# Performance work log

Hardware: AMD Instinct MI355X
Metric: run time of the kernel (lower is better)

Reference implementation:

```python
import jax, jax.numpy as jnp
import numpy as np

B, T, N, C_IN, C_HID, C_OUT = 1, 128, 50000, 16, 32, 8
E = 1_600_000
K = 2  # Chebyshev order


def setup_inputs() -> dict:
    key = jax.random.key(0)
    ks = jax.random.split(key, 12)
    X = jax.random.normal(ks[0], (B, T, N, C_IN), dtype=jnp.float32)
    edge_index = jax.random.randint(ks[1], (2, E), 0, N, dtype=jnp.int64)

    def mk_w(k, cin, cout):
        return jax.random.normal(k, (K, cin, cout), dtype=jnp.float32) / np.float32(np.sqrt(cin * K))

    inp = {"X": X, "edge_index": edge_index}
    names = ["xz", "hz", "xr", "hr", "xh", "hh"]
    for i, nm in enumerate(names):
        cin = C_IN if nm[0] == "x" else C_HID
        inp["W_" + nm] = mk_w(ks[2 + i], cin, C_HID)
        inp["b_" + nm] = jnp.zeros((C_HID,), jnp.float32)
    inp["fc_w"] = jax.random.normal(ks[10], (C_HID, C_OUT), jnp.float32) / np.float32(np.sqrt(C_HID))
    inp["fc_b"] = jnp.zeros((C_OUT,), jnp.float32)
    return inp


def _lap_edge_weights(edge_index, n):
    # ChebConv sym normalization with lambda_max=2: L_hat = -D^{-1/2} A D^{-1/2}, zero diag
    src, dst = edge_index[0], edge_index[1]
    deg = jax.ops.segment_sum(jnp.ones(src.shape, jnp.float32), src, num_segments=n)
    dinv = jnp.where(deg > 0, jax.lax.rsqrt(jnp.maximum(deg, 1.0)), 0.0)
    return -dinv[src] * dinv[dst]


def reference(X, edge_index, W_xz, b_xz, W_hz, b_hz, W_xr, b_xr, W_hr, b_hr,
              W_xh, b_xh, W_hh, b_hh, fc_w, fc_b):
    Ntot = B * N
    src, dst = edge_index[0], edge_index[1]
    w = _lap_edge_weights(edge_index, Ntot)  # [E]

    def agg(x):  # Tx_1 = L_hat @ x, irregular gather/scatter over edges
        return jax.ops.segment_sum(w[:, None] * x[src], dst, num_segments=Ntot)

    def cheb(x, W, b):  # K=2 Chebyshev conv
        return x @ W[0] + agg(x) @ W[1] + b

    def step(h, x_t):  # GConvGRU cell
        Z = jax.nn.sigmoid(cheb(x_t, W_xz, b_xz) + cheb(h, W_hz, b_hz))
        R = jax.nn.sigmoid(cheb(x_t, W_xr, b_xr) + cheb(h, W_hr, b_hr))
        Ht = jnp.tanh(cheb(x_t, W_xh, b_xh) + cheb(h * R, W_hh, b_hh))
        h = Z * h + (1.0 - Z) * Ht
        return h, h

    xs = jnp.swapaxes(X, 0, 1).reshape(T, Ntot, C_IN)  # [T, B*N, C_in]
    h0 = jnp.zeros((Ntot, C_HID), jnp.float32)
    _, hs = jax.lax.scan(step, h0, xs)                 # [T, B*N, H]
    outs = hs.reshape(T, B, N, C_HID).swapaxes(0, 1)   # [B, T, N, H]
    return outs @ fc_w + fc_b                           # [B, T, N, C_out]
```

## Files before the change

### kernel.cpp

```cpp
#include <hip/hip_runtime.h>
#include <cstdint>

#define NN   50000
#define TT   128
#define EE   1600000
#define CIN  16
#define CH   32
#define COUT 8

__device__ __forceinline__ float rlane(float v, int k) {
  return __int_as_float(__builtin_amdgcn_readlane(__float_as_int(v), k));
}
__device__ __forceinline__ float xhalf(float v) {
  return __shfl_xor(v, 32, 64);
}
__device__ __forceinline__ float sigf(float x) {
  return 1.0f / (1.0f + __expf(-x));
}
__device__ __forceinline__ float tanh_fast(float x) {
  x = fminf(fmaxf(x, -30.0f), 30.0f);
  float e = __expf(2.0f * x);
  return (e - 1.0f) / (e + 1.0f);
}

__global__ void k_flag(const int* __restrict__ idx, int* __restrict__ flag) {
  if (threadIdx.x == 0) {
    int m = 1;
    for (int i = 1; i <= 32; ++i)
      if (idx[2 * i + 1] != 0) m = 0;
    flag[0] = m;
  }
}

__global__ void k_zero_i(int* __restrict__ p, int n) {
  int i = blockIdx.x * blockDim.x + threadIdx.x;
  if (i < n) p[i] = 0;
}
__global__ void k_zero_f(float* __restrict__ p, int n) {
  int i = blockIdx.x * blockDim.x + threadIdx.x;
  if (i < n) p[i] = 0.0f;
}

__global__ void k_deg(const int* __restrict__ idx, int* __restrict__ deg_s,
                      int* __restrict__ deg_d, const int* __restrict__ flag) {
  int e = blockIdx.x * blockDim.x + threadIdx.x;
  if (e >= EE) return;
  int m = flag[0];
  int s = m ? idx[2 * e] : idx[e];
  int d = m ? idx[2 * (EE + e)] : idx[EE + e];
  atomicAdd(&deg_s[s], 1);
  atomicAdd(&deg_d[d], 1);
}

__global__ void k_dinv(const int* __restrict__ deg_s, float* __restrict__ dinv) {
  int i = blockIdx.x * blockDim.x + threadIdx.x;
  if (i < NN) {
    int d = deg_s[i];
    dinv[i] = (d > 0) ? rsqrtf((float)d) : 0.0f;
  }
}

__global__ void k_scan(const int* __restrict__ deg, int* __restrict__ row_ptr,
                       int* __restrict__ cursor) {
  __shared__ int part[1024];
  int tid = threadIdx.x;
  const int chunk = (NN + 1023) / 1024;
  int b = tid * chunk;
  int e = b + chunk; if (e > NN) e = NN;
  int s = 0;
  for (int j = b; j < e; ++j) s += deg[j];
  part[tid] = s;
  __syncthreads();
  for (int off = 1; off < 1024; off <<= 1) {
    int v = part[tid];
    int add = (tid >= off) ? part[tid - off] : 0;
    __syncthreads();
    part[tid] = v + add;
    __syncthreads();
  }
  int run = (tid > 0) ? part[tid - 1] : 0;
  for (int j = b; j < e; ++j) {
    row_ptr[j] = run; cursor[j] = run;
    run += deg[j];
  }
  if (tid == 1023) row_ptr[NN] = part[1023];
}

__global__ void k_fill(const int* __restrict__ idx, const float* __restrict__ dinv,
                       int* __restrict__ cursor, int* __restrict__ col,
                       float* __restrict__ wgt, const int* __restrict__ flag) {
  int e = blockIdx.x * blockDim.x + threadIdx.x;
  if (e >= EE) return;
  int m = flag[0];
  int s = m ? idx[2 * e] : idx[e];
  int d = m ? idx[2 * (EE + e)] : idx[EE + e];
  int p = atomicAdd(&cursor[d], 1);
  col[p] = s;
  wgt[p] = -dinv[s] * dinv[d];
}


__global__ __launch_bounds__(256, 4) void kx(
    const float* __restrict__ Xt,
    const int* __restrict__ row_ptr, const int* __restrict__ col,
    const float* __restrict__ wgt,
    const float* __restrict__ W_xz, const float* __restrict__ b_xz,
    const float* __restrict__ b_hz,
    const float* __restrict__ W_xr, const float* __restrict__ b_xr,
    const float* __restrict__ b_hr,
    const float* __restrict__ W_xh, const float* __restrict__ b_xh,
    const float* __restrict__ b_hh,
    float* __restrict__ Gx) {
  const int lane = threadIdx.x & 63;
  const int g = lane >> 5;
  const int c = lane & 31;
  const int ci = c & 15;
  const int wid = (blockIdx.x * blockDim.x + threadIdx.x) >> 6;
  const int nw = (gridDim.x * blockDim.x) >> 6;

  const float* Wzr = g ? W_xr : W_xz;
  float w0[CIN], w1[CIN], wh0[CIN], wh1[CIN];
#pragma unroll
  for (int k = 0; k < CIN; ++k) {
    w0[k]  = Wzr[k * CH + c];
    w1[k]  = Wzr[CIN * CH + k * CH + c];
    wh0[k] = W_xh[k * CH + c];
    wh1[k] = W_xh[CIN * CH + k * CH + c];
  }
  const float bzr = g ? (b_xr[c] + b_hr[c]) : (b_xz[c] + b_hz[c]);
  const float bh  = b_xh[c] + b_hh[c];

  for (int i = wid; i < NN; i += nw) {
    const int iu = __builtin_amdgcn_readfirstlane(i);
    const int e0 = __builtin_amdgcn_readfirstlane(row_ptr[iu]);
    const int e1 = __builtin_amdgcn_readfirstlane(row_ptr[iu + 1]);
    const int deg = e1 - e0;
    const int len0 = (deg + 1) >> 1;
    const int s = e0 + (g ? len0 : 0);
    const int send = g ? e1 : (e0 + len0);

    float a0 = 0.f, a1 = 0.f, a2 = 0.f, a3 = 0.f;
    int j = s;
    for (; j + 4 <= send; j += 4) {
      int s0 = col[j], s1 = col[j + 1], s2 = col[j + 2], s3 = col[j + 3];
      float wA = wgt[j], wB = wgt[j + 1], wC = wgt[j + 2], wD = wgt[j + 3];
      a0 += wA * Xt[s0 * CIN + ci];
      a1 += wB * Xt[s1 * CIN + ci];
      a2 += wC * Xt[s2 * CIN + ci];
      a3 += wD * Xt[s3 * CIN + ci];
    }
    for (; j < send; ++j)
      a0 += wgt[j] * Xt[col[j] * CIN + ci];
    float axh = (a0 + a1) + (a2 + a3);
    float ax = axh + xhalf(axh);

    const float* xrow = Xt + (size_t)iu * CIN;
    float accA = bzr, accH = bh;
#pragma unroll
    for (int k = 0; k < CIN; ++k) {
      float xk = xrow[k];
      float axk = rlane(ax, k);
      accA += xk * w0[k] + axk * w1[k];
      accH += xk * wh0[k] + axk * wh1[k];
    }
    float* grow = Gx + (size_t)iu * 96;
    grow[g * CH + c] = accA;
    if (g == 0) grow[64 + c] = accH;
  }
}

__global__ __launch_bounds__(256, 4) void k1(
    const float* __restrict__ h,
    const int* __restrict__ row_ptr, const int* __restrict__ col,
    const float* __restrict__ wgt,
    const float* __restrict__ W_hz, const float* __restrict__ W_hr,
    const float* __restrict__ Gx,
    float* __restrict__ Zb, float* __restrict__ hrb) {
  const int lane = threadIdx.x & 63;
  const int g = lane >> 5;
  const int c = lane & 31;
  const int wid = (blockIdx.x * blockDim.x + threadIdx.x) >> 6;
  const int nw = (gridDim.x * blockDim.x) >> 6;

  const float* Wh = g ? W_hr : W_hz;
  float w0[CH], w1[CH];
#pragma unroll
  for (int k = 0; k < CH; ++k) {
    w0[k] = Wh[k * CH + c];
    w1[k] = Wh[CH * CH + k * CH + c];
  }

  for (int i = wid; i < NN; i += nw) {
    const int iu = __builtin_amdgcn_readfirstlane(i);
    const int e0 = __builtin_amdgcn_readfirstlane(row_ptr[iu]);
    const int e1 = __builtin_amdgcn_readfirstlane(row_ptr[iu + 1]);
    const int deg = e1 - e0;
    const int len0 = (deg + 1) >> 1;
    const int s = e0 + (g ? len0 : 0);
    const int send = g ? e1 : (e0 + len0);

    float a0 = 0.f, a1 = 0.f, a2 = 0.f, a3 = 0.f;
    int j = s;
    for (; j + 4 <= send; j += 4) {
      int s0 = col[j], s1 = col[j + 1], s2 = col[j + 2], s3 = col[j + 3];
      float wA = wgt[j], wB = wgt[j + 1], wC = wgt[j + 2], wD = wgt[j + 3];
      a0 += wA * h[s0 * CH + c];
      a1 += wB * h[s1 * CH + c];
      a2 += wC * h[s2 * CH + c];
      a3 += wD * h[s3 * CH + c];
    }
    for (; j < send; ++j)
      a0 += wgt[j] * h[col[j] * CH + c];
    float ahh = (a0 + a1) + (a2 + a3);
    float ah = ahh + xhalf(ahh);

    const float* hrow = h + (size_t)iu * CH;
    float acc = Gx[(size_t)iu * 96 + g * CH + c];
#pragma unroll
    for (int k = 0; k < CH; ++k) {
      float hk = hrow[k];
      float ahk = rlane(ah, k);
      acc += hk * w0[k] + ahk * w1[k];
    }
    float sg = sigf(acc);
    float hv = hrow[c];
    if (g == 0) Zb[(size_t)iu * CH + c] = sg;
    else        hrb[(size_t)iu * CH + c] = hv * sg;
  }
}

__global__ __launch_bounds__(256, 4) void k2(
    float* __restrict__ h, const float* __restrict__ hrb,
    const int* __restrict__ row_ptr, const int* __restrict__ col,
    const float* __restrict__ wgt,
    const float* __restrict__ W_hh,
    const float* __restrict__ fc_w, const float* __restrict__ fc_b,
    const float* __restrict__ Gx, const float* __restrict__ Zb,
    float* __restrict__ outT) {
  const int lane = threadIdx.x & 63;
  const int g = lane >> 5;
  const int c = lane & 31;
  const int wid = (blockIdx.x * blockDim.x + threadIdx.x) >> 6;
  const int nw = (gridDim.x * blockDim.x) >> 6;

  float w0[CH], w1[CH], fcw[CH];
#pragma unroll
  for (int k = 0; k < CH; ++k) {
    w0[k] = W_hh[k * CH + c];
    w1[k] = W_hh[CH * CH + k * CH + c];
    fcw[k] = fc_w[k * COUT + (c & 7)];
  }
  const float fb = fc_b[c & 7];

  for (int i = wid; i < NN; i += nw) {
    const int iu = __builtin_amdgcn_readfirstlane(i);
    const int e0 = __builtin_amdgcn_readfirstlane(row_ptr[iu]);
    const int e1 = __builtin_amdgcn_readfirstlane(row_ptr[iu + 1]);
    const int deg = e1 - e0;
    const int len0 = (deg + 1) >> 1;
    const int s = e0 + (g ? len0 : 0);
    const int send = g ? e1 : (e0 + len0);

    float a0 = 0.f, a1 = 0.f, a2 = 0.f, a3 = 0.f;
    int j = s;
    for (; j + 4 <= send; j += 4) {
      int s0 = col[j], s1 = col[j + 1], s2 = col[j + 2], s3 = col[j + 3];
      float wA = wgt[j], wB = wgt[j + 1], wC = wgt[j + 2], wD = wgt[j + 3];
      a0 += wA * hrb[s0 * CH + c];
      a1 += wB * hrb[s1 * CH + c];
      a2 += wC * hrb[s2 * CH + c];
      a3 += wD * hrb[s3 * CH + c];
    }
    for (; j < send; ++j)
      a0 += wgt[j] * hrb[col[j] * CH + c];
    float ahh = (a0 + a1) + (a2 + a3);
    float ahr = ahh + xhalf(ahh);

    const float* hrrow = hrb + (size_t)iu * CH;
    const float* hrow = h + (size_t)iu * CH;
    float acc = Gx[(size_t)iu * 96 + 64 + c];
#pragma unroll
    for (int k = 0; k < CH; ++k) {
      float hk = hrrow[k];
      float ahk = rlane(ahr, k);
      acc += hk * w0[k] + ahk * w1[k];
    }
    float ht = tanh_fast(acc);
    float zv = Zb[(size_t)iu * CH + c];
    float hv = hrow[c];
    float hn = zv * hv + (1.0f - zv) * ht;
    if (g == 0) h[(size_t)iu * CH + c] = hn;

    float o0 = fb, o1 = 0.f;
#pragma unroll
    for (int k = 0; k < CH; k += 2) {
      o0 += rlane(hn, k) * fcw[k];
      o1 += rlane(hn, k + 1) * fcw[k + 1];
    }
    float o = o0 + o1;
    if (lane < COUT) outT[(size_t)iu * COUT + lane] = o;
  }
}

extern "C" void kernel_launch(void* const* d_in, const int* in_sizes, int n_in,
                              void* d_out, int out_size, void* d_ws, size_t ws_size,
                              hipStream_t stream) {
  const float* X = (const float*)d_in[0];
  const int* idx = (const int*)d_in[1];
  const float* W_xz = (const float*)d_in[2];  const float* b_xz = (const float*)d_in[3];
  const float* W_hz = (const float*)d_in[4];  const float* b_hz = (const float*)d_in[5];
  const float* W_xr = (const float*)d_in[6];  const float* b_xr = (const float*)d_in[7];
  const float* W_hr = (const float*)d_in[8];  const float* b_hr = (const float*)d_in[9];
  const float* W_xh = (const float*)d_in[10]; const float* b_xh = (const float*)d_in[11];
  const float* W_hh = (const float*)d_in[12]; const float* b_hh = (const float*)d_in[13];
  const float* fc_w = (const float*)d_in[14]; const float* fc_b = (const float*)d_in[15];
  float* out = (float*)d_out;

  char* ws = (char*)d_ws;
  size_t off = 0;
  auto alloc = [&](size_t bytes) -> void* {
    void* p = ws + off;
    off = (off + bytes + 255) & ~(size_t)255;
    return p;
  };
  int* flag = (int*)alloc(4);
  int* deg_s = (int*)alloc((size_t)NN * 4);
  int* deg_d = (int*)alloc((size_t)NN * 4);
  int* row_ptr = (int*)alloc((size_t)(NN + 1) * 4);
  int* cursor = (int*)alloc((size_t)NN * 4);
  float* dinv = (float*)alloc((size_t)NN * 4);
  int* col = (int*)alloc((size_t)EE * 4);
  float* wgt = (float*)alloc((size_t)EE * 4);
  float* h = (float*)alloc((size_t)NN * CH * 4);
  float* hrb = (float*)alloc((size_t)NN * CH * 4);
  float* Zb = (float*)alloc((size_t)NN * CH * 4);
  float* Gx = (float*)alloc((size_t)NN * 96 * 4);

  k_flag<<<1, 64, 0, stream>>>(idx, flag);
  k_zero_i<<<(NN + 255) / 256, 256, 0, stream>>>(deg_s, NN);
  k_zero_i<<<(NN + 255) / 256, 256, 0, stream>>>(deg_d, NN);
  k_deg<<<(EE + 255) / 256, 256, 0, stream>>>(idx, deg_s, deg_d, flag);
  k_dinv<<<(NN + 255) / 256, 256, 0, stream>>>(deg_s, dinv);
  k_scan<<<1, 1024, 0, stream>>>(deg_d, row_ptr, cursor);
  k_fill<<<(EE + 255) / 256, 256, 0, stream>>>(idx, dinv, cursor, col, wgt, flag);
  k_zero_f<<<(NN * CH + 255) / 256, 256, 0, stream>>>(h, NN * CH);

  const int blocks = 3125;
  for (int t = 0; t < TT; ++t) {
    const float* Xt = X + (size_t)t * NN * CIN;
    float* outT = out + (size_t)t * NN * COUT;
    kx<<<blocks, 256, 0, stream>>>(Xt, row_ptr, col, wgt,
                                   W_xz, b_xz, b_hz, W_xr, b_xr, b_hr,
                                   W_xh, b_xh, b_hh, Gx);
    k1<<<blocks, 256, 0, stream>>>(h, row_ptr, col, wgt, W_hz, W_hr, Gx, Zb, hrb);
    k2<<<blocks, 256, 0, stream>>>(h, hrb, row_ptr, col, wgt, W_hh,
                                   fc_w, fc_b, Gx, Zb, outT);
  }
}
```

Measured before the change: 26.84 ms.

## Hoist input-side Chebyshev convs out of time loop and batch gathers

Adds a single kx_all kernel that computes the input-side gate preactivations for all 128 timesteps up front, processing four timesteps per edge traversal so the col/wgt reads are shared. It is used when the workspace can hold a full T×N×96 buffer, and it removes the kx launch from the recurrent loop. The edge-gather loops in k1/k2 are rewritten to load 16 indices and weights at a time with a clamped tail, which exposes more memory-level parallelism. The recurrent kernels now process two nodes per wave iteration with launch bounds lowered to 3 waves per SIMD. The cost is a buffer of about 2.4 GB, plus extra memory traffic to write Gx for every timestep and read it back later.

```diff
diff --git a/kernel.cpp b/kernel.cpp
--- a/kernel.cpp
+++ b/kernel.cpp
@@ -21,6 +21,35 @@
   x = fminf(fmaxf(x, -30.0f), 30.0f);
   float e = __expf(2.0f * x);
   return (e - 1.0f) / (e + 1.0f);
+}
+
+__device__ __forceinline__ float agg16(const float* __restrict__ mat,
+                                       const int* __restrict__ col,
+                                       const float* __restrict__ wgt,
+                                       int e0, int e1, int g, int c) {
+  const int deg = e1 - e0;
+  const int len0 = (deg + 1) >> 1;
+  const int s = e0 + (g ? len0 : 0);
+  const int send = g ? e1 : (e0 + len0);
+  float a[4] = {0.f, 0.f, 0.f, 0.f};
+  int j = s;
+  while (j < send) {
+    int cidx[16];
+    float wv[16];
+#pragma unroll
+    for (int k = 0; k < 16; ++k) {
+      int jk = j + k;
+      int sj = (jk < send) ? jk : (send - 1);
+      cidx[k] = col[sj];
+      wv[k] = (jk < send) ? wgt[sj] : 0.0f;
+    }
+#pragma unroll
+    for (int k = 0; k < 16; ++k)
+      a[k & 3] += wv[k] * mat[(size_t)cidx[k] * CH + c];
+    j += 16;
+  }
+  float p = (a[0] + a[1]) + (a[2] + a[3]);
+  return p + xhalf(p);
 }
 
 __global__ void k_flag(const int* __restrict__ idx, int* __restrict__ flag) {
@@ -99,6 +128,84 @@
   wgt[p] = -dinv[s] * dinv[d];
 }
 
+__global__ __launch_bounds__(256, 3) void kx_all(
+    const float* __restrict__ X,
+    const int* __restrict__ row_ptr, const int* __restrict__ col,
+    const float* __restrict__ wgt,
+    const float* __restrict__ W_xz, const float* __restrict__ b_xz,
+    const float* __restrict__ b_hz,
+    const float* __restrict__ W_xr, const float* __restrict__ b_xr,
+    const float* __restrict__ b_hr,
+    const float* __restrict__ W_xh, const float* __restrict__ b_xh,
+    const float* __restrict__ b_hh,
+    float* __restrict__ Gx) {
+  const int lane = threadIdx.x & 63;
+  const int g = lane >> 5;
+  const int c = lane & 31;
+  const int ci = c & 15;
+  const int tq = blockIdx.x / 12500;
+  const int t0 = tq * 4;
+  const int node = (blockIdx.x % 12500) * 4 + (threadIdx.x >> 6);
+  const int iu = __builtin_amdgcn_readfirstlane(node);
+
+  const float* Wzr = g ? W_xr : W_xz;
+  float w0[CIN], w1[CIN], wh0[CIN], wh1[CIN];
+#pragma unroll
+  for (int k = 0; k < CIN; ++k) {
+    w0[k]  = Wzr[k * CH + c];
+    w1[k]  = Wzr[CIN * CH + k * CH + c];
+    wh0[k] = W_xh[k * CH + c];
+    wh1[k] = W_xh[CIN * CH + k * CH + c];
+  }
+  const float bzr = g ? (b_xr[c] + b_hr[c]) : (b_xz[c] + b_hz[c]);
+  const float bh  = b_xh[c] + b_hh[c];
+
+  const int e0 = __builtin_amdgcn_readfirstlane(row_ptr[iu]);
+  const int e1 = __builtin_amdgcn_readfirstlane(row_ptr[iu + 1]);
+  const int deg = e1 - e0;
+  const int len0 = (deg + 1) >> 1;
+  const int s = e0 + (g ? len0 : 0);
+  const int send = g ? e1 : (e0 + len0);
+
+  float ax4[4] = {0.f, 0.f, 0.f, 0.f};
+  int j = s;
+  for (; j + 4 <= send; j += 4) {
+    int c0 = col[j], c1 = col[j + 1], c2 = col[j + 2], c3 = col[j + 3];
+    float wA = wgt[j], wB = wgt[j + 1], wC = wgt[j + 2], wD = wgt[j + 3];
+#pragma unroll
+    for (int tp = 0; tp < 4; ++tp) {
+      const float* Xt = X + (size_t)(t0 + tp) * NN * CIN;
+      ax4[tp] += wA * Xt[c0 * CIN + ci] + wB * Xt[c1 * CIN + ci]
+               + wC * Xt[c2 * CIN + ci] + wD * Xt[c3 * CIN + ci];
+    }
+  }
+  for (; j < send; ++j) {
+    int cs = col[j];
+    float wv = wgt[j];
+#pragma unroll
+    for (int tp = 0; tp < 4; ++tp)
+      ax4[tp] += wv * (X + (size_t)(t0 + tp) * NN * CIN)[cs * CIN + ci];
+  }
+#pragma unroll
+  for (int tp = 0; tp < 4; ++tp)
+    ax4[tp] += xhalf(ax4[tp]);
+
+#pragma unroll
+  for (int tp = 0; tp < 4; ++tp) {
+    const float* xrow = X + ((size_t)(t0 + tp) * NN + iu) * CIN;
+    float accA = bzr, accH = bh;
+#pragma unroll
+    for (int k = 0; k < CIN; ++k) {
+      float xk = xrow[k];
+      float axk = rlane(ax4[tp], k);
+      accA += xk * w0[k] + axk * w1[k];
+      accH += xk * wh0[k] + axk * wh1[k];
+    }
+    float* grow = Gx + ((size_t)(t0 + tp) * NN + iu) * 96;
+    grow[g * CH + c] = accA;
+    if (g == 0) grow[64 + c] = accH;
+  }
+}
 
 __global__ __launch_bounds__(256, 4) void kx(
     const float* __restrict__ Xt,
@@ -138,20 +245,23 @@
     const int len0 = (deg + 1) >> 1;
     const int s = e0 + (g ? len0 : 0);
     const int send = g ? e1 : (e0 + len0);
-
-    float a0 = 0.f, a1 = 0.f, a2 = 0.f, a3 = 0.f;
+    float a[4] = {0.f, 0.f, 0.f, 0.f};
     int j = s;
-    for (; j + 4 <= send; j += 4) {
-      int s0 = col[j], s1 = col[j + 1], s2 = col[j + 2], s3 = col[j + 3];
-      float wA = wgt[j], wB = wgt[j + 1], wC = wgt[j + 2], wD = wgt[j + 3];
-      a0 += wA * Xt[s0 * CIN + ci];
-      a1 += wB * Xt[s1 * CIN + ci];
-      a2 += wC * Xt[s2 * CIN + ci];
-      a3 += wD * Xt[s3 * CIN + ci];
-    }
-    for (; j < send; ++j)
-      a0 += wgt[j] * Xt[col[j] * CIN + ci];
-    float axh = (a0 + a1) + (a2 + a3);
+    while (j < send) {
+      int cidx[16]; float wv[16];
+#pragma unroll
+      for (int k = 0; k < 16; ++k) {
+        int jk = j + k;
+        int sj = (jk < send) ? jk : (send - 1);
+        cidx[k] = col[sj];
+        wv[k] = (jk < send) ? wgt[sj] : 0.0f;
+      }
+#pragma unroll
+      for (int k = 0; k < 16; ++k)
+        a[k & 3] += wv[k] * Xt[(size_t)cidx[k] * CIN + ci];
+      j += 16;
+    }
+    float axh = (a[0] + a[1]) + (a[2] + a[3]);
     float ax = axh + xhalf(axh);
 
     const float* xrow = Xt + (size_t)iu * CIN;
@@ -169,12 +279,12 @@
   }
 }
 
-__global__ __launch_bounds__(256, 4) void k1(
+__global__ __launch_bounds__(256, 3) void k1(
     const float* __restrict__ h,
     const int* __restrict__ row_ptr, const int* __restrict__ col,
     const float* __restrict__ wgt,
     const float* __restrict__ W_hz, const float* __restrict__ W_hr,
-    const float* __restrict__ Gx,
+    const float* __restrict__ Gxt,
     float* __restrict__ Zb, float* __restrict__ hrb) {
   const int lane = threadIdx.x & 63;
   const int g = lane >> 5;
@@ -190,52 +300,37 @@
     w1[k] = Wh[CH * CH + k * CH + c];
   }
 
-  for (int i = wid; i < NN; i += nw) {
-    const int iu = __builtin_amdgcn_readfirstlane(i);
-    const int e0 = __builtin_amdgcn_readfirstlane(row_ptr[iu]);
-    const int e1 = __builtin_amdgcn_readfirstlane(row_ptr[iu + 1]);
-    const int deg = e1 - e0;
-    const int len0 = (deg + 1) >> 1;
-    const int s = e0 + (g ? len0 : 0);
-    const int send = g ? e1 : (e0 + len0);
-
-    float a0 = 0.f, a1 = 0.f, a2 = 0.f, a3 = 0.f;
-    int j = s;
-    for (; j + 4 <= send; j += 4) {
-      int s0 = col[j], s1 = col[j + 1], s2 = col[j + 2], s3 = col[j + 3];
-      float wA = wgt[j], wB = wgt[j + 1], wC = wgt[j + 2], wD = wgt[j + 3];
-      a0 += wA * h[s0 * CH + c];
-      a1 += wB * h[s1 * CH + c];
-      a2 += wC * h[s2 * CH + c];
-      a3 += wD * h[s3 * CH + c];
-    }
-    for (; j < send; ++j)
-      a0 += wgt[j] * h[col[j] * CH + c];
-    float ahh = (a0 + a1) + (a2 + a3);
-    float ah = ahh + xhalf(ahh);
-
-    const float* hrow = h + (size_t)iu * CH;
-    float acc = Gx[(size_t)iu * 96 + g * CH + c];
-#pragma unroll
-    for (int k = 0; k < CH; ++k) {
-      float hk = hrow[k];
-      float ahk = rlane(ah, k);
-      acc += hk * w0[k] + ahk * w1[k];
-    }
-    float sg = sigf(acc);
-    float hv = hrow[c];
-    if (g == 0) Zb[(size_t)iu * CH + c] = sg;
-    else        hrb[(size_t)iu * CH + c] = hv * sg;
-  }
-}
-
-__global__ __launch_bounds__(256, 4) void k2(
+  for (int i = wid * 2; i < NN; i += nw * 2) {
+#pragma unroll
+    for (int u = 0; u < 2; ++u) {
+      const int iu = __builtin_amdgcn_readfirstlane(i + u);
+      const int e0 = __builtin_amdgcn_readfirstlane(row_ptr[iu]);
+      const int e1 = __builtin_amdgcn_readfirstlane(row_ptr[iu + 1]);
+      float ah = agg16(h, col, wgt, e0, e1, g, c);
+
+      const float* hrow = h + (size_t)iu * CH;
+      float acc = Gxt[(size_t)iu * 96 + g * CH + c];
+#pragma unroll
+      for (int k = 0; k < CH; ++k) {
+        float hk = hrow[k];
+        float ahk = rlane(ah, k);
+        acc += hk * w0[k] + ahk * w1[k];
+      }
+      float sg = sigf(acc);
+      float hv = hrow[c];
+      if (g == 0) Zb[(size_t)iu * CH + c] = sg;
+      else        hrb[(size_t)iu * CH + c] = hv * sg;
+    }
+  }
+}
+
+__global__ __launch_bounds__(256, 3) void k2(
     float* __restrict__ h, const float* __restrict__ hrb,
     const int* __restrict__ row_ptr, const int* __restrict__ col,
     const float* __restrict__ wgt,
     const float* __restrict__ W_hh,
     const float* __restrict__ fc_w, const float* __restrict__ fc_b,
-    const float* __restrict__ Gx, const float* __restrict__ Zb,
+    const float* __restrict__ Gxt, const float* __restrict__ Zb,
     float* __restrict__ outT) {
   const int lane = threadIdx.x & 63;
   const int g = lane >> 5;
@@ -252,53 +347,38 @@
   }
   const float fb = fc_b[c & 7];
 
-  for (int i = wid; i < NN; i += nw) {
-    const int iu = __builtin_amdgcn_readfirstlane(i);
-    const int e0 = __builtin_amdgcn_readfirstlane(row_ptr[iu]);
-    const int e1 = __builtin_amdgcn_readfirstlane(row_ptr[iu + 1]);
-    const int deg = e1 - e0;
-    const int len0 = (deg + 1) >> 1;
-    const int s = e0 + (g ? len0 : 0);
-    const int send = g ? e1 : (e0 + len0);
-
-    float a0 = 0.f, a1 = 0.f, a2 = 0.f, a3 = 0.f;
-    int j = s;
-    for (; j + 4 <= send; j += 4) {
-      int s0 = col[j], s1 = col[j + 1], s2 = col[j + 2], s3 = col[j + 3];
-      float wA = wgt[j], wB = wgt[j + 1], wC = wgt[j + 2], wD = wgt[j + 3];
-      a0 += wA * hrb[s0 * CH + c];
-      a1 += wB * hrb[s1 * CH + c];
-      a2 += wC * hrb[s2 * CH + c];
-      a3 += wD * hrb[s3 * CH + c];
-    }
-    for (; j < send; ++j)
-      a0 += wgt[j] * hrb[col[j] * CH + c];
-    float ahh = (a0 + a1) + (a2 + a3);
-    float ahr = ahh + xhalf(ahh);
-
-    const float* hrrow = hrb + (size_t)iu * CH;
-    const float* hrow = h + (size_t)iu * CH;
-    float acc = Gx[(size_t)iu * 96 + 64 + c];
-#pragma unroll
-    for (int k = 0; k < CH; ++k) {
-      float hk = hrrow[k];
-      float ahk = rlane(ahr, k);
-      acc += hk * w0[k] + ahk * w1[k];
-    }
-    float ht = tanh_fast(acc);
-    float zv = Zb[(size_t)iu * CH + c];
-    float hv = hrow[c];
-    float hn = zv * hv + (1.0f - zv) * ht;
-    if (g == 0) h[(size_t)iu * CH + c] = hn;
-
-    float o0 = fb, o1 = 0.f;
-#pragma unroll
-    for (int k = 0; k < CH; k += 2) {
-      o0 += rlane(hn, k) * fcw[k];
-      o1 += rlane(hn, k + 1) * fcw[k + 1];
-    }
-    float o = o0 + o1;
-    if (lane < COUT) outT[(size_t)iu * COUT + lane] = o;
+  for (int i = wid * 2; i < NN; i += nw * 2) {
+#pragma unroll
+    for (int u = 0; u < 2; ++u) {
+      const int iu = __builtin_amdgcn_readfirstlane(i + u);
+      const int e0 = __builtin_amdgcn_readfirstlane(row_ptr[iu]);
+      const int e1 = __builtin_amdgcn_readfirstlane(row_ptr[iu + 1]);
+      float ahr = agg16(hrb, col, wgt, e0, e1, g, c);
+
+      const float* hrrow = hrb + (size_t)iu * CH;
+      const float* hrow = h + (size_t)iu * CH;
+      float acc = Gxt[(size_t)iu * 96 + 64 + c];
+#pragma unroll
+      for (int k = 0; k < CH; ++k) {
+        float hk = hrrow[k];
+        float ahk = rlane(ahr, k);
+        acc += hk * w0[k] + ahk * w1[k];
+      }
+      float ht = tanh_fast(acc);
+      float zv = Zb[(size_t)iu * CH + c];
+      float hv = hrow[c];
+      float hn = zv * hv + (1.0f - zv) * ht;
+      if (g == 0) h[(size_t)iu * CH + c] = hn;
+
+      float o0 = fb, o1 = 0.f;
+#pragma unroll
+      for (int k = 0; k < CH; k += 2) {
+        o0 += rlane(hn, k) * fcw[k];
+        o1 += rlane(hn, k + 1) * fcw[k + 1];
+      }
+      float o = o0 + o1;
+      if (lane < COUT) outT[(size_t)iu * COUT + lane] = o;
+    }
   }
 }
 
@@ -334,7 +414,11 @@
   float* h = (float*)alloc((size_t)NN * CH * 4);
   float* hrb = (float*)alloc((size_t)NN * CH * 4);
   float* Zb = (float*)alloc((size_t)NN * CH * 4);
-  float* Gx = (float*)alloc((size_t)NN * 96 * 4);
+
+  const size_t gx_step = (size_t)NN * 96;
+  const size_t gxall_bytes = (size_t)TT * gx_step * 4;
+  const bool full = (ws_size >= off + gxall_bytes + (1 << 20));
+  float* Gx = (float*)alloc(full ? gxall_bytes : gx_step * 4);
 
   k_flag<<<1, 64, 0, stream>>>(idx, flag);
   k_zero_i<<<(NN + 255) / 256, 256, 0, stream>>>(deg_s, NN);
@@ -345,15 +429,27 @@
   k_fill<<<(EE + 255) / 256, 256, 0, stream>>>(idx, dinv, cursor, col, wgt, flag);
   k_zero_f<<<(NN * CH + 255) / 256, 256, 0, stream>>>(h, NN * CH);
 
-  const int blocks = 3125;
+  if (full) {
+    kx_all<<<32 * 12500, 256, 0, stream>>>(X, row_ptr, col, wgt,
+                                           W_xz, b_xz, b_hz, W_xr, b_xr, b_hr,
+                                           W_xh, b_xh, b_hh, Gx);
+  }
+
+  const int rblocks = 6250;
   for (int t = 0; t < TT; ++t) {
-    const float* Xt = X + (size_t)t * NN * CIN;
     float* outT = out + (size_t)t * NN * COUT;
-    kx<<<blocks, 256, 0, stream>>>(Xt, row_ptr, col, wgt,
+    const float* Gxt;
+    if (full) {
+      Gxt = Gx + (size_t)t * gx_step;
+    } else {
+      const float* Xt = X + (size_t)t * NN * CIN;
+      kx<<<3125, 256, 0, stream>>>(Xt, row_ptr, col, wgt,
                                    W_xz, b_xz, b_hz, W_xr, b_xr, b_hr,
                                    W_xh, b_xh, b_hh, Gx);
-    k1<<<blocks, 256, 0, stream>>>(h, row_ptr, col, wgt, W_hz, W_hr, Gx, Zb, hrb);
-    k2<<<blocks, 256, 0, stream>>>(h, hrb, row_ptr, col, wgt, W_hh,
-                                   fc_w, fc_b, Gx, Zb, outT);
-  }
-}
+      Gxt = Gx;
+    }
+    k1<<<rblocks, 256, 0, stream>>>(h, row_ptr, col, wgt, W_hz, W_hr, Gxt, Zb, hrb);
+    k2<<<rblocks, 256, 0, stream>>>(h, hrb, row_ptr, col, wgt, W_hh,
+                                    fc_w, fc_b, Gxt, Zb, outT);
+  }
+}
```

Result: faster. 25.41 ms (-5.3%).
